# Performance work log

Measured on AMD Instinct MI355X. Metric: run time of the kernel, lower is better.

Reference implementation:

```python
import jax, jax.numpy as jnp
import numpy as np

N, F = 400000, 128
M = 100000
DENSE = [256, 256, 128]


def setup_inputs() -> dict:
    key = jax.random.key(0)
    ks = jax.random.split(key, 8)
    x = jax.random.normal(ks[0], (N, F), dtype=jnp.float32)
    sel_idx = jax.random.randint(ks[1], (M, 1), 0, N, dtype=jnp.int32)
    # Dense layer params, scaled like glorot-ish init
    W0 = jax.random.normal(ks[2], (F, DENSE[0]), dtype=jnp.float32) * (1.0 / np.sqrt(F))
    b0 = jnp.zeros((DENSE[0],), dtype=jnp.float32)
    W1 = jax.random.normal(ks[3], (DENSE[0], DENSE[1]), dtype=jnp.float32) * (1.0 / np.sqrt(DENSE[0]))
    b1 = jnp.zeros((DENSE[1],), dtype=jnp.float32)
    W2 = jax.random.normal(ks[4], (DENSE[1], DENSE[2]), dtype=jnp.float32) * (1.0 / np.sqrt(DENSE[1]))
    b2 = jnp.zeros((DENSE[2],), dtype=jnp.float32)
    return {"x": x, "sel_idx": sel_idx, "W0": W0, "b0": b0,
            "W1": W1, "b1": b1, "W2": W2, "b2": b2}


def reference(x, sel_idx, W0, b0, W1, b1, W2, b2):
    idx = sel_idx[:, 0]                       # [M]
    up = x[idx]                               # gather_nd -> [M, F]
    up = jax.nn.elu(up @ W0 + b0)             # [M, 256]
    up = jax.nn.elu(up @ W1 + b1)             # [M, 256]
    up = jax.nn.elu(up @ W2 + b2)             # [M, F]
    # x += scatter_nd(sel_idx, up, shape(x))
    return x + jnp.zeros_like(x).at[idx].add(up)
```

## Files before the change

### kernel.cpp

```cpp
#include <hip/hip_runtime.h>
#include <hip/hip_bf16.h>

#define NROWS 400000
#define MSEL  100000
#define FDIM  128
#define D0 256
#define D1 256
#define D2 128

typedef __attribute__((ext_vector_type(8))) short short8;
typedef __attribute__((ext_vector_type(4))) float f32x4;
typedef __attribute__((ext_vector_type(2))) unsigned int uint2v;

__device__ __forceinline__ unsigned short f2bf(float f) {
    unsigned int u = __float_as_uint(f);
    unsigned int r = (u + 0x7fffu + ((u >> 16) & 1u)) >> 16;
    return (unsigned short)r;
}

__device__ __forceinline__ unsigned int pk2bf(float a, float b) {
    __hip_bfloat162 h = __float22bfloat162_rn(make_float2(a, b));
    return *(unsigned int*)&h;
}

__device__ __forceinline__ float elu(float v) {
    return v > 0.f ? v : (__expf(v) - 1.f);
}

__global__ void prep1(const float* __restrict__ W0,
                      const float* __restrict__ W1,
                      const float* __restrict__ W2,
                      short* __restrict__ wp, int* __restrict__ head) {
    int bid = blockIdx.x;
    if (bid < 512) {
        int e = bid * 256 + threadIdx.x;
        const float* W; int N; int base; int le;
        if (e < 32768)       { W = W0; N = 256; base = 0;     le = e; }
        else if (e < 98304)  { W = W1; N = 256; base = 32768; le = e - 32768; }
        else                 { W = W2; N = 128; base = 98304; le = e - 98304; }
        int t    = le >> 9;
        int r    = le & 511;
        int lane = r >> 3;
        int j    = r & 7;
        int ntiles = N >> 4;
        int kt = t / ntiles, nt = t % ntiles;
        int k = kt * 32 + (lane >> 4) * 8 + j;
        int n = nt * 16 + (lane & 15);
        wp[base + le] = (short)f2bf(W[k * N + n]);
    } else {
        int i = (bid - 512) * 256 + threadIdx.x;
        if (i < NROWS) head[i] = -1;
    }
}

__global__ void prep2(const int* __restrict__ sel, const float* __restrict__ x,
                      int* __restrict__ head, int* __restrict__ next,
                      unsigned int* __restrict__ xf32) {
    int bid = blockIdx.x;
    if (bid < 391) {
        int j = bid * 256 + threadIdx.x;
        if (j < MSEL) next[j] = atomicExch(head + sel[j], j);
    } else {
        int g = (bid - 391) * 256 + threadIdx.x;
        int j = g >> 5, seg = g & 31;
        float4 v = ((const float4*)x)[(size_t)sel[j] * 32 + seg];
        int k0 = seg * 4;
        int lane = (j & 15) + ((k0 >> 3) & 3) * 16;
        int e = k0 & 7;
        int idx = ((((j >> 4) * 4 + (k0 >> 5)) * 512 + lane * 8 + e) >> 1);
        xf32[idx]     = pk2bf(v.x, v.y);
        xf32[idx + 1] = pk2bf(v.z, v.w);
    }
}

__global__ void copy_x(const float4* __restrict__ x, float4* __restrict__ out, int n4) {
    int i = blockIdx.x * blockDim.x + threadIdx.x;
    int stride = gridDim.x * blockDim.x;
    for (; i < n4; i += stride) out[i] = x[i];
}

template <bool SPLIT>
__global__ __launch_bounds__(256) void mlp_compute(
    const short* __restrict__ xf,
    const float* __restrict__ x, const int* __restrict__ sel,
    const short* __restrict__ wp,
    const float* __restrict__ b0v, const float* __restrict__ b1v,
    const float* __restrict__ b2v,
    unsigned short* __restrict__ upOut, float* __restrict__ out) {
    __shared__ __align__(16) short lds[16384];

    const int tid  = threadIdx.x;
    const int lane = tid & 63;
    const int w    = tid >> 6;
    const int rowBase = blockIdx.x * 32;
    const int lm = lane & 15;
    const int kq = lane >> 4;
    const int sxz = (lm & 7) << 3;

    const short* W0p = wp;
    const short* W1p = wp + 32768;
    const short* W2p = wp + 98304;

    short8 A0[2][4];
    if constexpr (SPLIT) {
        #pragma unroll
        for (int rt = 0; rt < 2; rt++)
            #pragma unroll
            for (int kt = 0; kt < 4; kt++)
                A0[rt][kt] = *(const short8*)(xf + (((size_t)blockIdx.x * 2 + rt) * 4 + kt) * 512 + lane * 8);
    }

    short8 B0[4][4];
    #pragma unroll
    for (int kt = 0; kt < 4; kt++)
        #pragma unroll
        for (int ntl = 0; ntl < 4; ntl++)
            B0[kt][ntl] = *(const short8*)(W0p + ((kt * 16 + (w * 4 + ntl)) * 512 + lane * 8));

    if constexpr (!SPLIT) {
        const float4* xv = (const float4*)x;
        #pragma unroll
        for (int it = 0; it < 4; it++) {
            int i = it * 256 + tid;
            int row = i >> 5, seg = i & 31;
            float4 v = xv[(size_t)sel[rowBase + row] * 32 + seg];
            uint2v p = { pk2bf(v.x, v.y), pk2bf(v.z, v.w) };
            *(uint2v*)(&lds[8192 + ((row * 128 + seg * 4) ^ ((row & 7) << 3))]) = p;
        }
        __syncthreads();
    }

    const f32x4 zero4 = {0.f, 0.f, 0.f, 0.f};

    short8 B1a[8][2];
    {
        f32x4 acc[2][4];
        #pragma unroll
        for (int i = 0; i < 2; i++)
            #pragma unroll
            for (int j = 0; j < 4; j++) acc[i][j] = zero4;
        #pragma unroll
        for (int rt = 0; rt < 2; rt++) {
            short8 a[4];
            #pragma unroll
            for (int kt = 0; kt < 4; kt++) {
                if constexpr (SPLIT) a[kt] = A0[rt][kt];
                else {
                    int rowA = rt * 16 + lm;
                    a[kt] = *(const short8*)(&lds[8192 + ((rowA * 128 + kt * 32 + kq * 8) ^ sxz)]);
                }
            }
            #pragma unroll
            for (int ntl = 0; ntl < 4; ntl++)
                #pragma unroll
                for (int kt = 0; kt < 4; kt++)
                    acc[rt][ntl] = __builtin_amdgcn_mfma_f32_16x16x32_bf16(a[kt], B0[kt][ntl], acc[rt][ntl], 0, 0, 0);
        }
        #pragma unroll
        for (int kt = 0; kt < 8; kt++)
            #pragma unroll
            for (int p = 0; p < 2; p++)
                B1a[kt][p] = *(const short8*)(W1p + ((kt * 16 + (w * 4 + p)) * 512 + lane * 8));

        #pragma unroll
        for (int ntl = 0; ntl < 4; ntl++) {
            int col = (w * 4 + ntl) * 16 + lm;
            float bias = b0v[col];
            #pragma unroll
            for (int rt = 0; rt < 2; rt++) {
                float v0 = elu(acc[rt][ntl][0] + bias);
                float v1 = elu(acc[rt][ntl][1] + bias);
                float v2 = elu(acc[rt][ntl][2] + bias);
                float v3 = elu(acc[rt][ntl][3] + bias);
                unsigned int u01 = pk2bf(v0, v1), u23 = pk2bf(v2, v3);
                int row = rt * 16 + kq * 4;
                lds[(((row+0) * 256 + col) ^ (((row+0) & 7) << 3))] = (short)(u01 & 0xffff);
                lds[(((row+1) * 256 + col) ^ (((row+1) & 7) << 3))] = (short)(u01 >> 16);
                lds[(((row+2) * 256 + col) ^ (((row+2) & 7) << 3))] = (short)(u23 & 0xffff);
                lds[(((row+3) * 256 + col) ^ (((row+3) & 7) << 3))] = (short)(u23 >> 16);
            }
        }
    }
    __syncthreads();

    short8 B2[8][2];
    {
        short8 B1b[8][2];
        #pragma unroll
        for (int kt = 0; kt < 8; kt++)
            #pragma unroll
            for (int p = 0; p < 2; p++)
                B1b[kt][p] = *(const short8*)(W1p + ((kt * 16 + (w * 4 + 2 + p)) * 512 + lane * 8));

        f32x4 acc[2][2];
        #pragma unroll
        for (int i = 0; i < 2; i++)
            #pragma unroll
            for (int j = 0; j < 2; j++) acc[i][j] = zero4;
        #pragma unroll
        for (int rt = 0; rt < 2; rt++) {
            short8 a[8];
            int rowA = rt * 16 + lm;
            #pragma unroll
            for (int kt = 0; kt < 8; kt++)
                a[kt] = *(const short8*)(&lds[(rowA * 256 + kt * 32 + kq * 8) ^ sxz]);
            #pragma unroll
            for (int p = 0; p < 2; p++)
                #pragma unroll
                for (int kt = 0; kt < 8; kt++)
                    acc[rt][p] = __builtin_amdgcn_mfma_f32_16x16x32_bf16(a[kt], B1a[kt][p], acc[rt][p], 0, 0, 0);
        }
        #pragma unroll
        for (int p = 0; p < 2; p++) {
            int col = (w * 4 + p) * 16 + lm;
            float bias = b1v[col];
            #pragma unroll
            for (int rt = 0; rt < 2; rt++) {
                float v0 = elu(acc[rt][p][0] + bias);
                float v1 = elu(acc[rt][p][1] + bias);
                float v2 = elu(acc[rt][p][2] + bias);
                float v3 = elu(acc[rt][p][3] + bias);
                unsigned int u01 = pk2bf(v0, v1), u23 = pk2bf(v2, v3);
                int row = rt * 16 + kq * 4;
                lds[8192 + (((row+0) * 256 + col) ^ (((row+0) & 7) << 3))] = (short)(u01 & 0xffff);
                lds[8192 + (((row+1) * 256 + col) ^ (((row+1) & 7) << 3))] = (short)(u01 >> 16);
                lds[8192 + (((row+2) * 256 + col) ^ (((row+2) & 7) << 3))] = (short)(u23 & 0xffff);
                lds[8192 + (((row+3) * 256 + col) ^ (((row+3) & 7) << 3))] = (short)(u23 >> 16);
            }
        }

        #pragma unroll
        for (int i = 0; i < 2; i++)
            #pragma unroll
            for (int j = 0; j < 2; j++) acc[i][j] = zero4;
        #pragma unroll
        for (int rt = 0; rt < 2; rt++) {
            short8 a[8];
            int rowA = rt * 16 + lm;
            #pragma unroll
            for (int kt = 0; kt < 8; kt++)
                a[kt] = *(const short8*)(&lds[(rowA * 256 + kt * 32 + kq * 8) ^ sxz]);
            #pragma unroll
            for (int p = 0; p < 2; p++)
                #pragma unroll
                for (int kt = 0; kt < 8; kt++)
                    acc[rt][p] = __builtin_amdgcn_mfma_f32_16x16x32_bf16(a[kt], B1b[kt][p], acc[rt][p], 0, 0, 0);
        }
        #pragma unroll
        for (int kt = 0; kt < 8; kt++)
            #pragma unroll
            for (int ntl = 0; ntl < 2; ntl++)
                B2[kt][ntl] = *(const short8*)(W2p + ((kt * 8 + (w * 2 + ntl)) * 512 + lane * 8));

        #pragma unroll
        for (int p = 0; p < 2; p++) {
            int col = (w * 4 + 2 + p) * 16 + lm;
            float bias = b1v[col];
            #pragma unroll
            for (int rt = 0; rt < 2; rt++) {
                float v0 = elu(acc[rt][p][0] + bias);
                float v1 = elu(acc[rt][p][1] + bias);
                float v2 = elu(acc[rt][p][2] + bias);
                float v3 = elu(acc[rt][p][3] + bias);
                unsigned int u01 = pk2bf(v0, v1), u23 = pk2bf(v2, v3);
                int row = rt * 16 + kq * 4;
                lds[8192 + (((row+0) * 256 + col) ^ (((row+0) & 7) << 3))] = (short)(u01 & 0xffff);
                lds[8192 + (((row+1) * 256 + col) ^ (((row+1) & 7) << 3))] = (short)(u01 >> 16);
                lds[8192 + (((row+2) * 256 + col) ^ (((row+2) & 7) << 3))] = (short)(u23 & 0xffff);
                lds[8192 + (((row+3) * 256 + col) ^ (((row+3) & 7) << 3))] = (short)(u23 >> 16);
            }
        }
    }
    __syncthreads();

    {
        f32x4 acc[2][2];
        #pragma unroll
        for (int i = 0; i < 2; i++)
            #pragma unroll
            for (int j = 0; j < 2; j++) acc[i][j] = zero4;
        #pragma unroll
        for (int rt = 0; rt < 2; rt++) {
            short8 a[8];
            int rowA = rt * 16 + lm;
            #pragma unroll
            for (int kt = 0; kt < 8; kt++)
                a[kt] = *(const short8*)(&lds[8192 + ((rowA * 256 + kt * 32 + kq * 8) ^ sxz)]);
            #pragma unroll
            for (int ntl = 0; ntl < 2; ntl++)
                #pragma unroll
                for (int kt = 0; kt < 8; kt++)
                    acc[rt][ntl] = __builtin_amdgcn_mfma_f32_16x16x32_bf16(a[kt], B2[kt][ntl], acc[rt][ntl], 0, 0, 0);
        }
        #pragma unroll
        for (int ntl = 0; ntl < 2; ntl++) {
            int col = (w * 2 + ntl) * 16 + lm;
            float bias = b2v[col];
            #pragma unroll
            for (int rt = 0; rt < 2; rt++)
                #pragma unroll
                for (int r = 0; r < 4; r++) {
                    int row = rt * 16 + kq * 4 + r;
                    float v = elu(acc[rt][ntl][r] + bias);
                    if (SPLIT) {
                        lds[row * 128 + col] = (short)f2bf(v);
                    } else {
                        atomicAdd(out + (size_t)sel[rowBase + row] * 128 + col, v);
                    }
                }
        }
    }
    if (SPLIT) {
        __syncthreads();
        const short8* s8 = (const short8*)(&lds[0]);
        short8* u8 = (short8*)(upOut + (size_t)rowBase * 128);
        u8[tid]       = s8[tid];
        u8[tid + 256] = s8[tid + 256];
    }
}

__global__ __launch_bounds__(256) void merge_out(
    const float2* __restrict__ x2, const unsigned int* __restrict__ up32,
    const int* __restrict__ head, const int* __restrict__ next,
    float2* __restrict__ out2) {
    int wid  = blockIdx.x * 4 + (threadIdx.x >> 6);
    int lane = threadIdx.x & 63;
    int wstride = gridDim.x * 4;
    for (int row = wid; row < NROWS; row += wstride) {
        float2 v = x2[(size_t)row * 64 + lane];
        int j = head[row];
        while (j >= 0) {
            unsigned int u = up32[(size_t)j * 64 + lane];
            v.x += __uint_as_float(u << 16);
            v.y += __uint_as_float(u & 0xffff0000u);
            j = next[j];
        }
        out2[(size_t)row * 64 + lane] = v;
    }
}

extern "C" void kernel_launch(void* const* d_in, const int* in_sizes, int n_in,
                              void* d_out, int out_size, void* d_ws, size_t ws_size,
                              hipStream_t stream) {
    const float* x   = (const float*)d_in[0];
    const int*   sel = (const int*)d_in[1];
    const float* W0  = (const float*)d_in[2];
    const float* b0  = (const float*)d_in[3];
    const float* W1  = (const float*)d_in[4];
    const float* b1  = (const float*)d_in[5];
    const float* W2  = (const float*)d_in[6];
    const float* b2  = (const float*)d_in[7];
    float* out = (float*)d_out;

    char* wsb = (char*)d_ws;
    short* wp          = (short*)wsb;
    short* xf          = (short*)(wsb + 262144);
    unsigned short* up = (unsigned short*)(wsb + 262144 + 25600000);
    int* head          = (int*)(wsb + 262144 + 51200000);
    int* nxt           = head + NROWS;
    const size_t need  = 262144 + 51200000 + (size_t)NROWS * 4 + (size_t)MSEL * 4;

    prep1<<<2075, 256, 0, stream>>>(W0, W1, W2, wp, head);
    if (ws_size >= need) {
        prep2<<<12891, 256, 0, stream>>>(sel, x, head, nxt, (unsigned int*)xf);
        mlp_compute<true><<<MSEL / 32, 256, 0, stream>>>(xf, x, sel, wp, b0, b1, b2, up, out);
        merge_out<<<4096, 256, 0, stream>>>((const float2*)x, (const unsigned int*)up,
                                            head, nxt, (float2*)out);
    } else {
        copy_x<<<4096, 256, 0, stream>>>((const float4*)x, (float4*)out, NROWS * FDIM / 4);
        mlp_compute<false><<<MSEL / 32, 256, 0, stream>>>(xf, x, sel, wp, b0, b1, b2, up, out);
    }
}
```

Before: 152.0 us.

## Use 64-row, 512-thread MLP blocks and merge prep kernels into one launch

The MLP kernel now processes 64 selected rows per block with 8 waves instead of 32 rows with 4. Each wave owns fewer output columns, so each weight fragment loaded into registers is reused across twice as many rows. Layer-0 A-fragment loads are software-pipelined against the MFMAs, and W1/W2 weights are loaded in K-halves to reduce register pressure. The two prep kernels are fused into one launch, with the head initialisation moved to a hipMemsetAsync. In exchange, LDS per block doubles, fewer blocks run per CU, and the tail block needs bounds clamping.

```diff
diff --git a/kernel.cpp b/kernel.cpp
--- a/kernel.cpp
+++ b/kernel.cpp
@@ -4,9 +4,6 @@
 #define NROWS 400000
 #define MSEL  100000
 #define FDIM  128
-#define D0 256
-#define D1 256
-#define D2 128
 
 typedef __attribute__((ext_vector_type(8))) short short8;
 typedef __attribute__((ext_vector_type(4))) float f32x4;
@@ -27,10 +24,11 @@
     return v > 0.f ? v : (__expf(v) - 1.f);
 }
 
-__global__ void prep1(const float* __restrict__ W0,
-                      const float* __restrict__ W1,
-                      const float* __restrict__ W2,
-                      short* __restrict__ wp, int* __restrict__ head) {
+__global__ void prep(const float* __restrict__ W0, const float* __restrict__ W1,
+                     const float* __restrict__ W2, short* __restrict__ wp,
+                     const int* __restrict__ sel, const float* __restrict__ x,
+                     int* __restrict__ head, int* __restrict__ next,
+                     unsigned int* __restrict__ xf32) {
     int bid = blockIdx.x;
     if (bid < 512) {
         int e = bid * 256 + threadIdx.x;
@@ -47,21 +45,11 @@
         int k = kt * 32 + (lane >> 4) * 8 + j;
         int n = nt * 16 + (lane & 15);
         wp[base + le] = (short)f2bf(W[k * N + n]);
-    } else {
-        int i = (bid - 512) * 256 + threadIdx.x;
-        if (i < NROWS) head[i] = -1;
-    }
-}
-
-__global__ void prep2(const int* __restrict__ sel, const float* __restrict__ x,
-                      int* __restrict__ head, int* __restrict__ next,
-                      unsigned int* __restrict__ xf32) {
-    int bid = blockIdx.x;
-    if (bid < 391) {
-        int j = bid * 256 + threadIdx.x;
+    } else if (bid < 903) {
+        int j = (bid - 512) * 256 + threadIdx.x;
         if (j < MSEL) next[j] = atomicExch(head + sel[j], j);
     } else {
-        int g = (bid - 391) * 256 + threadIdx.x;
+        int g = (bid - 903) * 256 + threadIdx.x;
         int j = g >> 5, seg = g & 31;
         float4 v = ((const float4*)x)[(size_t)sel[j] * 32 + seg];
         int k0 = seg * 4;
@@ -80,19 +68,19 @@
 }
 
 template <bool SPLIT>
-__global__ __launch_bounds__(256) void mlp_compute(
+__global__ __launch_bounds__(512) void mlp_compute(
     const short* __restrict__ xf,
     const float* __restrict__ x, const int* __restrict__ sel,
     const short* __restrict__ wp,
     const float* __restrict__ b0v, const float* __restrict__ b1v,
     const float* __restrict__ b2v,
     unsigned short* __restrict__ upOut, float* __restrict__ out) {
-    __shared__ __align__(16) short lds[16384];
+    __shared__ __align__(16) short lds[32768];
 
     const int tid  = threadIdx.x;
     const int lane = tid & 63;
     const int w    = tid >> 6;
-    const int rowBase = blockIdx.x * 32;
+    const int rowBase = blockIdx.x * 64;
     const int lm = lane & 15;
     const int kq = lane >> 4;
     const int sxz = (lm & 7) << 3;
@@ -101,222 +89,176 @@
     const short* W1p = wp + 32768;
     const short* W2p = wp + 98304;
 
-    short8 A0[2][4];
-    if constexpr (SPLIT) {
-        #pragma unroll
-        for (int rt = 0; rt < 2; rt++)
-            #pragma unroll
-            for (int kt = 0; kt < 4; kt++)
-                A0[rt][kt] = *(const short8*)(xf + (((size_t)blockIdx.x * 2 + rt) * 4 + kt) * 512 + lane * 8);
-    }
-
-    short8 B0[4][4];
+    const f32x4 zero4 = {0.f, 0.f, 0.f, 0.f};
+
+    short8 aA[4], aB[4];
+    const int g0 = blockIdx.x * 4;
+#define A0LD(dst, rt) { int rg_ = g0 + (rt); if (rg_ > MSEL/16 - 1) rg_ = MSEL/16 - 1; \
+    _Pragma("unroll") for (int kt_ = 0; kt_ < 4; kt_++) \
+        dst[kt_] = *(const short8*)(xf + ((size_t)rg_ * 4 + kt_) * 512 + lane * 8); }
+    if constexpr (SPLIT) { A0LD(aA, 0); A0LD(aB, 1); }
+
+    short8 B0[4][2];
     #pragma unroll
     for (int kt = 0; kt < 4; kt++)
         #pragma unroll
-        for (int ntl = 0; ntl < 4; ntl++)
-            B0[kt][ntl] = *(const short8*)(W0p + ((kt * 16 + (w * 4 + ntl)) * 512 + lane * 8));
+        for (int ntl = 0; ntl < 2; ntl++)
+            B0[kt][ntl] = *(const short8*)(W0p + ((kt * 16 + (w * 2 + ntl)) * 512 + lane * 8));
 
     if constexpr (!SPLIT) {
         const float4* xv = (const float4*)x;
         #pragma unroll
         for (int it = 0; it < 4; it++) {
-            int i = it * 256 + tid;
+            int i = it * 512 + tid;
             int row = i >> 5, seg = i & 31;
-            float4 v = xv[(size_t)sel[rowBase + row] * 32 + seg];
+            int j = rowBase + row; if (j >= MSEL) j = rowBase;
+            float4 v = xv[(size_t)sel[j] * 32 + seg];
             uint2v p = { pk2bf(v.x, v.y), pk2bf(v.z, v.w) };
-            *(uint2v*)(&lds[8192 + ((row * 128 + seg * 4) ^ ((row & 7) << 3))]) = p;
+            *(uint2v*)(&lds[16384 + ((row * 128 + seg * 4) ^ ((row & 7) << 3))]) = p;
         }
         __syncthreads();
     }
 
-    const f32x4 zero4 = {0.f, 0.f, 0.f, 0.f};
-
-    short8 B1a[8][2];
+    f32x4 acc0[4][2];
+    #pragma unroll
+    for (int i = 0; i < 4; i++) { acc0[i][0] = zero4; acc0[i][1] = zero4; }
+
+#define L0T(rt, ab) { _Pragma("unroll") for (int ntl_ = 0; ntl_ < 2; ntl_++) \
+    _Pragma("unroll") for (int kt_ = 0; kt_ < 4; kt_++) \
+        acc0[rt][ntl_] = __builtin_amdgcn_mfma_f32_16x16x32_bf16(ab[kt_], B0[kt_][ntl_], acc0[rt][ntl_], 0, 0, 0); }
+#define L0TL(rt) { short8 a_[4]; int rowA_ = (rt) * 16 + lm; \
+    _Pragma("unroll") for (int kt_ = 0; kt_ < 4; kt_++) \
+        a_[kt_] = *(const short8*)(&lds[16384 + ((rowA_ * 128 + kt_ * 32 + kq * 8) ^ sxz)]); \
+    _Pragma("unroll") for (int ntl_ = 0; ntl_ < 2; ntl_++) \
+    _Pragma("unroll") for (int kt_ = 0; kt_ < 4; kt_++) \
+        acc0[rt][ntl_] = __builtin_amdgcn_mfma_f32_16x16x32_bf16(a_[kt_], B0[kt_][ntl_], acc0[rt][ntl_], 0, 0, 0); }
+
+    if constexpr (SPLIT) {
+        L0T(0, aA); A0LD(aA, 2);
+        L0T(1, aB); A0LD(aB, 3);
+        L0T(2, aA);
+        L0T(3, aB);
+    } else {
+        L0TL(0); L0TL(1); L0TL(2); L0TL(3);
+    }
+
+    #pragma unroll
+    for (int ntl = 0; ntl < 2; ntl++) {
+        int col = (w * 2 + ntl) * 16 + lm;
+        float bias = b0v[col];
+        #pragma unroll
+        for (int rt = 0; rt < 4; rt++) {
+            float v0 = elu(acc0[rt][ntl][0] + bias);
+            float v1 = elu(acc0[rt][ntl][1] + bias);
+            float v2 = elu(acc0[rt][ntl][2] + bias);
+            float v3 = elu(acc0[rt][ntl][3] + bias);
+            unsigned int u01 = pk2bf(v0, v1), u23 = pk2bf(v2, v3);
+            int row = rt * 16 + kq * 4;
+            lds[(((row+0) * 256 + col) ^ (((row+0) & 7) << 3))] = (short)(u01 & 0xffff);
+            lds[(((row+1) * 256 + col) ^ (((row+1) & 7) << 3))] = (short)(u01 >> 16);
+            lds[(((row+2) * 256 + col) ^ (((row+2) & 7) << 3))] = (short)(u23 & 0xffff);
+            lds[(((row+3) * 256 + col) ^ (((row+3) & 7) << 3))] = (short)(u23 >> 16);
+        }
+    }
+    __syncthreads();
+
+    f32x4 acc1[4][2];
+    #pragma unroll
+    for (int i = 0; i < 4; i++) { acc1[i][0] = zero4; acc1[i][1] = zero4; }
+    #pragma unroll
+    for (int kh = 0; kh < 2; kh++) {
+        short8 Bh[4][2];
+        #pragma unroll
+        for (int kk = 0; kk < 4; kk++)
+            #pragma unroll
+            for (int ntl = 0; ntl < 2; ntl++)
+                Bh[kk][ntl] = *(const short8*)(W1p + (((kh * 4 + kk) * 16 + (w * 2 + ntl)) * 512 + lane * 8));
+        #pragma unroll
+        for (int rt = 0; rt < 4; rt++) {
+            short8 a[4];
+            int rowA = rt * 16 + lm;
+            #pragma unroll
+            for (int kk = 0; kk < 4; kk++)
+                a[kk] = *(const short8*)(&lds[(rowA * 256 + (kh * 4 + kk) * 32 + kq * 8) ^ sxz]);
+            #pragma unroll
+            for (int ntl = 0; ntl < 2; ntl++)
+                #pragma unroll
+                for (int kk = 0; kk < 4; kk++)
+                    acc1[rt][ntl] = __builtin_amdgcn_mfma_f32_16x16x32_bf16(a[kk], Bh[kk][ntl], acc1[rt][ntl], 0, 0, 0);
+        }
+    }
+    #pragma unroll
+    for (int ntl = 0; ntl < 2; ntl++) {
+        int col = (w * 2 + ntl) * 16 + lm;
+        float bias = b1v[col];
+        #pragma unroll
+        for (int rt = 0; rt < 4; rt++) {
+            float v0 = elu(acc1[rt][ntl][0] + bias);
+            float v1 = elu(acc1[rt][ntl][1] + bias);
+            float v2 = elu(acc1[rt][ntl][2] + bias);
+            float v3 = elu(acc1[rt][ntl][3] + bias);
+            unsigned int u01 = pk2bf(v0, v1), u23 = pk2bf(v2, v3);
+            int row = rt * 16 + kq * 4;
+            lds[16384 + (((row+0) * 256 + col) ^ (((row+0) & 7) << 3))] = (short)(u01 & 0xffff);
+            lds[16384 + (((row+1) * 256 + col) ^ (((row+1) & 7) << 3))] = (short)(u01 >> 16);
+            lds[16384 + (((row+2) * 256 + col) ^ (((row+2) & 7) << 3))] = (short)(u23 & 0xffff);
+            lds[16384 + (((row+3) * 256 + col) ^ (((row+3) & 7) << 3))] = (short)(u23 >> 16);
+        }
+    }
+    __syncthreads();
+
+    f32x4 acc2[4];
+    #pragma unroll
+    for (int i = 0; i < 4; i++) acc2[i] = zero4;
+    #pragma unroll
+    for (int kh = 0; kh < 2; kh++) {
+        short8 Bh[4];
+        #pragma unroll
+        for (int kk = 0; kk < 4; kk++)
+            Bh[kk] = *(const short8*)(W2p + (((kh * 4 + kk) * 8 + w) * 512 + lane * 8));
+        #pragma unroll
+        for (int rt = 0; rt < 4; rt++) {
+            short8 a[4];
+            int rowA = rt * 16 + lm;
+            #pragma unroll
+            for (int kk = 0; kk < 4; kk++)
+                a[kk] = *(const short8*)(&lds[16384 + ((rowA * 256 + (kh * 4 + kk) * 32 + kq * 8) ^ sxz)]);
+            #pragma unroll
+            for (int kk = 0; kk < 4; kk++)
+                acc2[rt] = __builtin_amdgcn_mfma_f32_16x16x32_bf16(a[kk], Bh[kk], acc2[rt], 0, 0, 0);
+        }
+    }
     {
-        f32x4 acc[2][4];
-        #pragma unroll
-        for (int i = 0; i < 2; i++)
-            #pragma unroll
-            for (int j = 0; j < 4; j++) acc[i][j] = zero4;
-        #pragma unroll
-        for (int rt = 0; rt < 2; rt++) {
-            short8 a[4];
-            #pragma unroll
-            for (int kt = 0; kt < 4; kt++) {
-                if constexpr (SPLIT) a[kt] = A0[rt][kt];
-                else {
-                    int rowA = rt * 16 + lm;
-                    a[kt] = *(const short8*)(&lds[8192 + ((rowA * 128 + kt * 32 + kq * 8) ^ sxz)]);
+        int col = w * 16 + lm;
+        float bias = b2v[col];
+        #pragma unroll
+        for (int rt = 0; rt < 4; rt++)
+            #pragma unroll
+            for (int r = 0; r < 4; r++) {
+                int row = rt * 16 + kq * 4 + r;
+                float v = elu(acc2[rt][r] + bias);
+                if (SPLIT) {
+                    lds[row * 128 + col] = (short)f2bf(v);
+                } else {
+                    int j = rowBase + row;
+                    if (j < MSEL) atomicAdd(out + (size_t)sel[j] * 128 + col, v);
                 }
             }
-            #pragma unroll
-            for (int ntl = 0; ntl < 4; ntl++)
-                #pragma unroll
-                for (int kt = 0; kt < 4; kt++)
-                    acc[rt][ntl] = __builtin_amdgcn_mfma_f32_16x16x32_bf16(a[kt], B0[kt][ntl], acc[rt][ntl], 0, 0, 0);
-        }
-        #pragma unroll
-        for (int kt = 0; kt < 8; kt++)
-            #pragma unroll
-            for (int p = 0; p < 2; p++)
-                B1a[kt][p] = *(const short8*)(W1p + ((kt * 16 + (w * 4 + p)) * 512 + lane * 8));
-
-        #pragma unroll
-        for (int ntl = 0; ntl < 4; ntl++) {
-            int col = (w * 4 + ntl) * 16 + lm;
-            float bias = b0v[col];
-            #pragma unroll
-            for (int rt = 0; rt < 2; rt++) {
-                float v0 = elu(acc[rt][ntl][0] + bias);
-                float v1 = elu(acc[rt][ntl][1] + bias);
-                float v2 = elu(acc[rt][ntl][2] + bias);
-                float v3 = elu(acc[rt][ntl][3] + bias);
-                unsigned int u01 = pk2bf(v0, v1), u23 = pk2bf(v2, v3);
-                int row = rt * 16 + kq * 4;
-                lds[(((row+0) * 256 + col) ^ (((row+0) & 7) << 3))] = (short)(u01 & 0xffff);
-                lds[(((row+1) * 256 + col) ^ (((row+1) & 7) << 3))] = (short)(u01 >> 16);
-                lds[(((row+2) * 256 + col) ^ (((row+2) & 7) << 3))] = (short)(u23 & 0xffff);
-                lds[(((row+3) * 256 + col) ^ (((row+3) & 7) << 3))] = (short)(u23 >> 16);
-            }
-        }
-    }
-    __syncthreads();
-
-    short8 B2[8][2];
-    {
-        short8 B1b[8][2];
-        #pragma unroll
-        for (int kt = 0; kt < 8; kt++)
-            #pragma unroll
-            for (int p = 0; p < 2; p++)
-                B1b[kt][p] = *(const short8*)(W1p + ((kt * 16 + (w * 4 + 2 + p)) * 512 + lane * 8));
-
-        f32x4 acc[2][2];
-        #pragma unroll
-        for (int i = 0; i < 2; i++)
-            #pragma unroll
-            for (int j = 0; j < 2; j++) acc[i][j] = zero4;
-        #pragma unroll
-        for (int rt = 0; rt < 2; rt++) {
-            short8 a[8];
-            int rowA = rt * 16 + lm;
-            #pragma unroll
-            for (int kt = 0; kt < 8; kt++)
-                a[kt] = *(const short8*)(&lds[(rowA * 256 + kt * 32 + kq * 8) ^ sxz]);
-            #pragma unroll
-            for (int p = 0; p < 2; p++)
-                #pragma unroll
-                for (int kt = 0; kt < 8; kt++)
-                    acc[rt][p] = __builtin_amdgcn_mfma_f32_16x16x32_bf16(a[kt], B1a[kt][p], acc[rt][p], 0, 0, 0);
-        }
-        #pragma unroll
-        for (int p = 0; p < 2; p++) {
-            int col = (w * 4 + p) * 16 + lm;
-            float bias = b1v[col];
-            #pragma unroll
-            for (int rt = 0; rt < 2; rt++) {
-                float v0 = elu(acc[rt][p][0] + bias);
-                float v1 = elu(acc[rt][p][1] + bias);
-                float v2 = elu(acc[rt][p][2] + bias);
-                float v3 = elu(acc[rt][p][3] + bias);
-                unsigned int u01 = pk2bf(v0, v1), u23 = pk2bf(v2, v3);
-                int row = rt * 16 + kq * 4;
-                lds[8192 + (((row+0) * 256 + col) ^ (((row+0) & 7) << 3))] = (short)(u01 & 0xffff);
-                lds[8192 + (((row+1) * 256 + col) ^ (((row+1) & 7) << 3))] = (short)(u01 >> 16);
-                lds[8192 + (((row+2) * 256 + col) ^ (((row+2) & 7) << 3))] = (short)(u23 & 0xffff);
-                lds[8192 + (((row+3) * 256 + col) ^ (((row+3) & 7) << 3))] = (short)(u23 >> 16);
-            }
-        }
-
-        #pragma unroll
-        for (int i = 0; i < 2; i++)
-            #pragma unroll
-            for (int j = 0; j < 2; j++) acc[i][j] = zero4;
-        #pragma unroll
-        for (int rt = 0; rt < 2; rt++) {
-            short8 a[8];
-            int rowA = rt * 16 + lm;
-            #pragma unroll
-            for (int kt = 0; kt < 8; kt++)
-                a[kt] = *(const short8*)(&lds[(rowA * 256 + kt * 32 + kq * 8) ^ sxz]);
-            #pragma unroll
-            for (int p = 0; p < 2; p++)
-                #pragma unroll
-                for (int kt = 0; kt < 8; kt++)
-                    acc[rt][p] = __builtin_amdgcn_mfma_f32_16x16x32_bf16(a[kt], B1b[kt][p], acc[rt][p], 0, 0, 0);
-        }
-        #pragma unroll
-        for (int kt = 0; kt < 8; kt++)
-            #pragma unroll
-            for (int ntl = 0; ntl < 2; ntl++)
-                B2[kt][ntl] = *(const short8*)(W2p + ((kt * 8 + (w * 2 + ntl)) * 512 + lane * 8));
-
-        #pragma unroll
-        for (int p = 0; p < 2; p++) {
-            int col = (w * 4 + 2 + p) * 16 + lm;
-            float bias = b1v[col];
-            #pragma unroll
-            for (int rt = 0; rt < 2; rt++) {
-                float v0 = elu(acc[rt][p][0] + bias);
-                float v1 = elu(acc[rt][p][1] + bias);
-                float v2 = elu(acc[rt][p][2] + bias);
-                float v3 = elu(acc[rt][p][3] + bias);
-                unsigned int u01 = pk2bf(v0, v1), u23 = pk2bf(v2, v3);
-                int row = rt * 16 + kq * 4;
-                lds[8192 + (((row+0) * 256 + col) ^ (((row+0) & 7) << 3))] = (short)(u01 & 0xffff);
-                lds[8192 + (((row+1) * 256 + col) ^ (((row+1) & 7) << 3))] = (short)(u01 >> 16);
-                lds[8192 + (((row+2) * 256 + col) ^ (((row+2) & 7) << 3))] = (short)(u23 & 0xffff);
-                lds[8192 + (((row+3) * 256 + col) ^ (((row+3) & 7) << 3))] = (short)(u23 >> 16);
-            }
-        }
-    }
-    __syncthreads();
-
-    {
-        f32x4 acc[2][2];
-        #pragma unroll
-        for (int i = 0; i < 2; i++)
-            #pragma unroll
-            for (int j = 0; j < 2; j++) acc[i][j] = zero4;
-        #pragma unroll
-        for (int rt = 0; rt < 2; rt++) {
-            short8 a[8];
-            int rowA = rt * 16 + lm;
-            #pragma unroll
-            for (int kt = 0; kt < 8; kt++)
-                a[kt] = *(const short8*)(&lds[8192 + ((rowA * 256 + kt * 32 + kq * 8) ^ sxz)]);
-            #pragma unroll
-            for (int ntl = 0; ntl < 2; ntl++)
-                #pragma unroll
-                for (int kt = 0; kt < 8; kt++)
-                    acc[rt][ntl] = __builtin_amdgcn_mfma_f32_16x16x32_bf16(a[kt], B2[kt][ntl], acc[rt][ntl], 0, 0, 0);
-        }
-        #pragma unroll
-        for (int ntl = 0; ntl < 2; ntl++) {
-            int col = (w * 2 + ntl) * 16 + lm;
-            float bias = b2v[col];
-            #pragma unroll
-            for (int rt = 0; rt < 2; rt++)
-                #pragma unroll
-                for (int r = 0; r < 4; r++) {
-                    int row = rt * 16 + kq * 4 + r;
-                    float v = elu(acc[rt][ntl][r] + bias);
-                    if (SPLIT) {
-                        lds[row * 128 + col] = (short)f2bf(v);
-                    } else {
-                        atomicAdd(out + (size_t)sel[rowBase + row] * 128 + col, v);
-                    }
-                }
-        }
     }
     if (SPLIT) {
         __syncthreads();
         const short8* s8 = (const short8*)(&lds[0]);
-        short8* u8 = (short8*)(upOut + (size_t)rowBase * 128);
-        u8[tid]       = s8[tid];
-        u8[tid + 256] = s8[tid + 256];
-    }
+        short8* u8 = (short8*)upOut;
+        #pragma unroll
+        for (int i = 0; i < 2; i++) {
+            int idx = i * 512 + tid;
+            int gg = blockIdx.x * 1024 + idx;
+            if (gg < MSEL * 16) u8[gg] = s8[idx];
+        }
+    }
+#undef A0LD
+#undef L0T
+#undef L0TL
 }
 
 __global__ __launch_bounds__(256) void merge_out(
@@ -360,14 +302,19 @@
     int* nxt           = head + NROWS;
     const size_t need  = 262144 + 51200000 + (size_t)NROWS * 4 + (size_t)MSEL * 4;
 
-    prep1<<<2075, 256, 0, stream>>>(W0, W1, W2, wp, head);
     if (ws_size >= need) {
-        prep2<<<12891, 256, 0, stream>>>(sel, x, head, nxt, (unsigned int*)xf);
-        mlp_compute<true><<<MSEL / 32, 256, 0, stream>>>(xf, x, sel, wp, b0, b1, b2, up, out);
+        hipMemsetAsync(head, 0xFF, (size_t)NROWS * 4, stream);
+        prep<<<13403, 256, 0, stream>>>(W0, W1, W2, wp, sel, x, head, nxt,
+                                        (unsigned int*)xf);
+        mlp_compute<true><<<(MSEL + 63) / 64, 512, 0, stream>>>(
+            xf, x, sel, wp, b0, b1, b2, up, out);
         merge_out<<<4096, 256, 0, stream>>>((const float2*)x, (const unsigned int*)up,
                                             head, nxt, (float2*)out);
     } else {
+        prep<<<512, 256, 0, stream>>>(W0, W1, W2, wp, sel, x, head, nxt,
+                                      (unsigned int*)xf);
         copy_x<<<4096, 256, 0, stream>>>((const float4*)x, (float4*)out, NROWS * FDIM / 4);
-        mlp_compute<false><<<MSEL / 32, 256, 0, stream>>>(xf, x, sel, wp, b0, b1, b2, up, out);
-    }
-}
+        mlp_compute<false><<<(MSEL + 63) / 64, 512, 0, stream>>>(
+            xf, x, sel, wp, b0, b1, b2, up, out);
+    }
+}
```

After: 151.1 us. About the same (-0.6%).
